# Optimization experiments

Measured on AMD Instinct MI355X. Metric: run time of the kernel, lower is better.

The kernel has to match this reference:

```python
import jax, jax.numpy as jnp
import numpy as np
import math

N_NODES = 50000
N_EDGES = 800000
D = 128
ALPHA = 0.1
BETA = 0.5


def setup_inputs() -> dict:
    key = jax.random.key(0)
    k = jax.random.split(key, 7)
    h = jax.random.normal(k[0], (N_NODES, D), dtype=jnp.float32)
    h0 = jax.random.normal(k[1], (N_NODES, D), dtype=jnp.float32)
    edge_row = jnp.sort(jax.random.randint(k[2], (N_EDGES,), 0, N_NODES, dtype=jnp.int32))
    edge_col = jax.random.randint(k[3], (N_EDGES,), 0, N_NODES, dtype=jnp.int32)
    edge_vals = jax.random.uniform(k[4], (N_EDGES,), dtype=jnp.float32)
    # nn.Linear(input_dim, output_dim): W is [out, in], b is [out]
    bound = 1.0 / math.sqrt(D)
    W = jax.random.uniform(k[5], (D, D), minval=-bound, maxval=bound, dtype=jnp.float32)
    b = jax.random.uniform(k[6], (D,), minval=-bound, maxval=bound, dtype=jnp.float32)
    return {"h": h, "h0": h0, "edge_row": edge_row, "edge_col": edge_col,
            "edge_vals": edge_vals, "W": W, "b": b, "l": 4}


def reference(h, h0, edge_row, edge_col, edge_vals, W, b, l):
    theta = math.log(BETA / l + 1.0)
    # sparse adj @ h : gather source features, scale by edge value, scatter-add to rows
    msgs = edge_vals[:, None] * h[edge_col]          # [E, D]
    hi = jax.ops.segment_sum(msgs, edge_row, num_segments=N_NODES)  # [N, D]
    support = (1.0 - ALPHA) * hi + ALPHA * h0
    lin = support @ W.T + b
    return theta * lin + (1.0 - theta) * support
```

## Files before the change

### kernel.cpp

```cpp
#include <hip/hip_runtime.h>
#include <hip/hip_bf16.h>
#include <math.h>

#define NN 50000
#define DD 128
#define ALPHA 0.1f
#define BETA 0.5f

typedef __attribute__((ext_vector_type(8))) short short8;
typedef __attribute__((ext_vector_type(4))) float floatx4;
typedef _Float16 h2 __attribute__((ext_vector_type(2)));

__device__ __forceinline__ float bf16lo(unsigned u) {
    return __uint_as_float(u << 16);
}
__device__ __forceinline__ float bf16hi(unsigned u) {
    return __uint_as_float(u & 0xffff0000u);
}
__device__ __forceinline__ unsigned pkh(float a, float b) {
    h2 p = {(_Float16)a, (_Float16)b};
    return __builtin_bit_cast(unsigned, p);
}
__device__ __forceinline__ h2 as_h2(unsigned u) {
    return __builtin_bit_cast(h2, u);
}

__global__ __launch_bounds__(256) void prep_kernel(
    const int* __restrict__ edge_row, int E, int* __restrict__ rp,
    const float* __restrict__ h, ushort* __restrict__ hh,
    const float* __restrict__ W, ushort* __restrict__ wf)
{
    const int t = blockIdx.x * 256 + threadIdx.x;

    if (hh != nullptr && t < NN * DD / 8) {
        const float4 v0 = *reinterpret_cast<const float4*>(h + (size_t)t * 8);
        const float4 v1 = *reinterpret_cast<const float4*>(h + (size_t)t * 8 + 4);
        uint4 o;
        o.x = pkh(v0.x, v0.y);
        o.y = pkh(v0.z, v0.w);
        o.z = pkh(v1.x, v1.y);
        o.w = pkh(v1.z, v1.w);
        *reinterpret_cast<uint4*>(hh + (size_t)t * 8) = o;
    }

    if (wf != nullptr && t < DD * DD / 4) {
        const float4 v = *reinterpret_cast<const float4*>(W + (size_t)t * 4);
        uint2 of;
        of.x = pkh(v.x, v.y);
        of.y = pkh(v.z, v.w);
        *reinterpret_cast<uint2*>(wf + (size_t)t * 4) = of;
    }

    if (t <= E) {
        if (t == 0) {
            int r0 = edge_row[0];
            for (int r = 0; r <= r0; ++r) rp[r] = 0;
        } else if (t == E) {
            int rl = edge_row[E - 1];
            for (int r = rl + 1; r <= NN; ++r) rp[r] = E;
        } else {
            int rprev = edge_row[t - 1];
            int rcur  = edge_row[t];
            for (int r = rprev + 1; r <= rcur; ++r) rp[r] = t;
        }
    }
}

__global__ __launch_bounds__(1024, 8) void fused16w(
    const ushort* __restrict__ hh, const float* __restrict__ h0,
    const int* __restrict__ edge_col, const float* __restrict__ edge_vals,
    const int* __restrict__ rp, const ushort* __restrict__ wf,
    const float* __restrict__ b, const int* __restrict__ lptr,
    float* __restrict__ out)
{
    __shared__ ushort sA[16][136];

    const int tid  = threadIdx.x;
    const int wave = tid >> 6;
    const int lane = tid & 63;
    const int g    = lane >> 4;
    const int li   = lane & 15;
    const int r0   = blockIdx.x * 16;
    const int r    = r0 + wave;

    const int lv = *lptr;
    const float theta  = logf(BETA / (float)lv + 1.0f);
    const float mtheta = 1.0f - theta;

    const int e0 = rp[r], e1 = rp[r + 1];

    h2 a0 = {0, 0}, a1 = {0, 0}, a2 = {0, 0}, a3 = {0, 0};

    for (int eb = e0; eb < e1; eb += 16) {
        #pragma unroll
        for (int u = 0; u < 4; ++u) {
            const int e  = eb + u * 4 + g;
            const int ee = min(e, e1 - 1);
            const int   c = edge_col[ee];
            const float v = (e < e1) ? edge_vals[ee] : 0.0f;
            const uint4 hv = *reinterpret_cast<const uint4*>(
                hh + (size_t)c * DD + li * 8);
            const _Float16 vh = (_Float16)v;
            const h2 vv = {vh, vh};
            a0 += as_h2(hv.x) * vv;
            a1 += as_h2(hv.y) * vv;
            a2 += as_h2(hv.z) * vv;
            a3 += as_h2(hv.w) * vv;
        }
    }

    float acc[8];
    acc[0] = (float)a0.x; acc[1] = (float)a0.y;
    acc[2] = (float)a1.x; acc[3] = (float)a1.y;
    acc[4] = (float)a2.x; acc[5] = (float)a2.y;
    acc[6] = (float)a3.x; acc[7] = (float)a3.y;

    #pragma unroll
    for (int j = 0; j < 8; ++j) {
        acc[j] += __shfl_xor(acc[j], 16);
        acc[j] += __shfl_xor(acc[j], 32);
    }

    if (g == 0) {
        const float4 h0a = *reinterpret_cast<const float4*>(
            h0 + (size_t)r * DD + li * 8);
        const float4 h0b = *reinterpret_cast<const float4*>(
            h0 + (size_t)r * DD + li * 8 + 4);
        float sup[8];
        sup[0] = fmaf(1.0f - ALPHA, acc[0], ALPHA * h0a.x);
        sup[1] = fmaf(1.0f - ALPHA, acc[1], ALPHA * h0a.y);
        sup[2] = fmaf(1.0f - ALPHA, acc[2], ALPHA * h0a.z);
        sup[3] = fmaf(1.0f - ALPHA, acc[3], ALPHA * h0a.w);
        sup[4] = fmaf(1.0f - ALPHA, acc[4], ALPHA * h0b.x);
        sup[5] = fmaf(1.0f - ALPHA, acc[5], ALPHA * h0b.y);
        sup[6] = fmaf(1.0f - ALPHA, acc[6], ALPHA * h0b.z);
        sup[7] = fmaf(1.0f - ALPHA, acc[7], ALPHA * h0b.w);
        uint4 pk;
        pk.x = pkh(sup[0], sup[1]);
        pk.y = pkh(sup[2], sup[3]);
        pk.z = pkh(sup[4], sup[5]);
        pk.w = pkh(sup[6], sup[7]);
        *reinterpret_cast<uint4*>(&sA[wave][li * 8]) = pk;
    }
    __syncthreads();

    if (wave >= 8) return;

    const int la = lane & 15;
    const int k0 = (lane >> 4) * 8;
    const int c  = wave * 16 + la;

    floatx4 facc = (floatx4){0.f, 0.f, 0.f, 0.f};

    #pragma unroll
    for (int s = 0; s < 4; ++s) {
        const int k = s * 32 + k0;
        const short8 af = *reinterpret_cast<const short8*>(&sA[la][k]);
        const short8 bf = *reinterpret_cast<const short8*>(
            wf + (size_t)c * DD + k);
        facc = __builtin_amdgcn_mfma_f32_16x16x32_f16(af, bf, facc, 0, 0, 0);
    }

    const int rg = (lane >> 4) * 4;
    const float bb = b[c];
    #pragma unroll
    for (int j = 0; j < 4; ++j) {
        const int rl = rg + j;
        const float sup = (float)(*reinterpret_cast<const _Float16*>(&sA[rl][c]));
        out[(size_t)(r0 + rl) * DD + c] =
            theta * (facc[j] + bb) + mtheta * sup;
    }
}

__global__ __launch_bounds__(256, 6) void agg_fp32(
    const float* __restrict__ h, const float* __restrict__ h0,
    const int* __restrict__ edge_col, const float* __restrict__ edge_vals,
    const int* __restrict__ rp, float* __restrict__ io)
{
    const int wave = threadIdx.x >> 6;
    const int lane = threadIdx.x & 63;
    const int p    = lane >> 5;
    const int li   = lane & 31;
    const int r    = blockIdx.x * 4 + wave;
    if (r >= NN) return;

    const int e0 = rp[r], e1 = rp[r + 1];

    float4 A[4];
    #pragma unroll
    for (int u = 0; u < 4; ++u) A[u] = make_float4(0.f, 0.f, 0.f, 0.f);

    for (int eb = e0; eb < e1; eb += 8) {
        #pragma unroll
        for (int u = 0; u < 4; ++u) {
            const int e  = eb + 2 * u + p;
            const int ee = min(e, e1 - 1);
            const int   c = edge_col[ee];
            const float v = (e < e1) ? edge_vals[ee] : 0.0f;
            const float4 hv =
                *reinterpret_cast<const float4*>(h + (size_t)c * DD + li * 4);
            A[u].x = fmaf(v, hv.x, A[u].x);
            A[u].y = fmaf(v, hv.y, A[u].y);
            A[u].z = fmaf(v, hv.z, A[u].z);
            A[u].w = fmaf(v, hv.w, A[u].w);
        }
    }
    float4 s;
    s.x = (A[0].x + A[1].x) + (A[2].x + A[3].x);
    s.y = (A[0].y + A[1].y) + (A[2].y + A[3].y);
    s.z = (A[0].z + A[1].z) + (A[2].z + A[3].z);
    s.w = (A[0].w + A[1].w) + (A[2].w + A[3].w);
    s.x += __shfl_xor(s.x, 32);
    s.y += __shfl_xor(s.y, 32);
    s.z += __shfl_xor(s.z, 32);
    s.w += __shfl_xor(s.w, 32);

    if (p == 0) {
        const float4 h0v =
            *reinterpret_cast<const float4*>(h0 + (size_t)r * DD + li * 4);
        float4 sup;
        sup.x = fmaf(1.0f - ALPHA, s.x, ALPHA * h0v.x);
        sup.y = fmaf(1.0f - ALPHA, s.y, ALPHA * h0v.y);
        sup.z = fmaf(1.0f - ALPHA, s.z, ALPHA * h0v.z);
        sup.w = fmaf(1.0f - ALPHA, s.w, ALPHA * h0v.w);
        *reinterpret_cast<float4*>(io + (size_t)r * DD + li * 4) = sup;
    }
}

#define RPB 64
#define SPAD 132
#define WPAD 136

__global__ __launch_bounds__(512, 4) void lin_kernel(
    float* io, const float* __restrict__ W, const float* __restrict__ b,
    const int* __restrict__ lptr)
{
    __shared__ float sS[RPB][SPAD];
    __shared__ __hip_bfloat16 sWt[DD][WPAD];

    const int tid = threadIdx.x;
    const int r0  = blockIdx.x * RPB;
    const int tr  = tid >> 4;
    const int tc  = tid & 15;

    const int lv = *lptr;
    const float theta  = logf(BETA / (float)lv + 1.0f);
    const float mtheta = 1.0f - theta;

    for (int i = tid * 4; i < DD * DD; i += 512 * 4) {
        const float4 w4 = *reinterpret_cast<const float4*>(W + i);
        const int o = i >> 7;
        const int k = i & 127;
        sWt[k + 0][o] = __float2bfloat16(w4.x);
        sWt[k + 1][o] = __float2bfloat16(w4.y);
        sWt[k + 2][o] = __float2bfloat16(w4.z);
        sWt[k + 3][o] = __float2bfloat16(w4.w);
    }

    for (int idx = tid; idx < RPB * 32; idx += 512) {
        const int row = idx >> 5;
        const int q   = idx & 31;
        const int rr  = r0 + row;
        const float4 v = (rr < NN)
            ? *reinterpret_cast<const float4*>(io + (size_t)rr * DD + q * 4)
            : make_float4(0.f, 0.f, 0.f, 0.f);
        *reinterpret_cast<float4*>(&sS[row][q * 4]) = v;
    }
    __syncthreads();

    float acc[2][8];
    #pragma unroll
    for (int i = 0; i < 2; ++i)
        #pragma unroll
        for (int j = 0; j < 8; ++j) acc[i][j] = 0.f;

    for (int k = 0; k < DD; k += 4) {
        const float4 a0 = *reinterpret_cast<const float4*>(&sS[tr * 2 + 0][k]);
        const float4 a1 = *reinterpret_cast<const float4*>(&sS[tr * 2 + 1][k]);
        const float aa0[4] = {a0.x, a0.y, a0.z, a0.w};
        const float aa1[4] = {a1.x, a1.y, a1.z, a1.w};
        #pragma unroll
        for (int kk = 0; kk < 4; ++kk) {
            const uint4 wr = *reinterpret_cast<const uint4*>(&sWt[k + kk][tc * 8]);
            float w[8];
            w[0] = bf16lo(wr.x); w[1] = bf16hi(wr.x);
            w[2] = bf16lo(wr.y); w[3] = bf16hi(wr.y);
            w[4] = bf16lo(wr.z); w[5] = bf16hi(wr.z);
            w[6] = bf16lo(wr.w); w[7] = bf16hi(wr.w);
            #pragma unroll
            for (int j = 0; j < 8; ++j) {
                acc[0][j] = fmaf(aa0[kk], w[j], acc[0][j]);
                acc[1][j] = fmaf(aa1[kk], w[j], acc[1][j]);
            }
        }
    }

    #pragma unroll
    for (int i = 0; i < 2; ++i) {
        const int ri = tr * 2 + i;
        const int rr = r0 + ri;
        if (rr >= NN) continue;
        #pragma unroll
        for (int j4 = 0; j4 < 2; ++j4) {
            const int cc = tc * 8 + j4 * 4;
            const float4 bv  = *reinterpret_cast<const float4*>(&b[cc]);
            const float4 sup = *reinterpret_cast<const float4*>(&sS[ri][cc]);
            float4 o4;
            o4.x = theta * (acc[i][j4 * 4 + 0] + bv.x) + mtheta * sup.x;
            o4.y = theta * (acc[i][j4 * 4 + 1] + bv.y) + mtheta * sup.y;
            o4.z = theta * (acc[i][j4 * 4 + 2] + bv.z) + mtheta * sup.z;
            o4.w = theta * (acc[i][j4 * 4 + 3] + bv.w) + mtheta * sup.w;
            *reinterpret_cast<float4*>(io + (size_t)rr * DD + cc) = o4;
        }
    }
}

extern "C" void kernel_launch(void* const* d_in, const int* in_sizes, int n_in,
                              void* d_out, int out_size, void* d_ws, size_t ws_size,
                              hipStream_t stream) {
    const float* h         = (const float*)d_in[0];
    const float* h0        = (const float*)d_in[1];
    const int*   edge_row  = (const int*)d_in[2];
    const int*   edge_col  = (const int*)d_in[3];
    const float* edge_vals = (const float*)d_in[4];
    const float* W         = (const float*)d_in[5];
    const float* b         = (const float*)d_in[6];
    const int*   lptr      = (const int*)d_in[7];
    const int E = in_sizes[2];

    char* wsb = (char*)d_ws;
    const size_t sz_hh = (size_t)NN * DD * sizeof(ushort);
    const size_t sz_w  = (size_t)DD * DD * sizeof(ushort);
    int*    rp = (int*)wsb;
    ushort* hh = (ushort*)(wsb + (1 << 18));
    ushort* wf = (ushort*)(wsb + (1 << 18) + sz_hh);
    float*  io = (float*)d_out;

    const size_t need = (size_t)(1 << 18) + sz_hh + sz_w;

    const int nT = (NN * DD / 8 > E + 1) ? NN * DD / 8 : E + 1;
    const int gridP = (nT + 255) / 256;

    if (ws_size >= need) {
        prep_kernel<<<gridP, 256, 0, stream>>>(edge_row, E, rp, h, hh, W, wf);
        fused16w<<<NN / 16, 1024, 0, stream>>>(
            hh, h0, edge_col, edge_vals, rp, wf, b, lptr, io);
    } else {
        prep_kernel<<<gridP, 256, 0, stream>>>(edge_row, E, rp, h,
                                               nullptr, W, nullptr);
        agg_fp32<<<(NN + 3) / 4, 256, 0, stream>>>(h, h0, edge_col, edge_vals, rp, io);
        lin_kernel<<<(NN + RPB - 1) / RPB, 512, 0, stream>>>(io, W, b, lptr);
    }
}
```

Measured before the change: 66.46 us.

## Process two rows per wave in fused aggregation kernel with 512-thread blocks

Changes the fused SpMM+linear kernel from 16 waves per block (one row each) to 8 waves per block with each wave aggregating two rows at once. This interleaves the gather loads for two rows to raise memory-level parallelism per wave. It also removes the idle half of the block during the MFMA phase, since all 8 waves now do the GEMM. The trade-off is load imbalance between paired rows: the loop runs to the longer of the two edge lists. It also uses more registers per wave.

```diff
diff --git a/kernel.cpp b/kernel.cpp
--- a/kernel.cpp
+++ b/kernel.cpp
@@ -66,7 +66,7 @@
     }
 }
 
-__global__ __launch_bounds__(1024, 8) void fused16w(
+__global__ __launch_bounds__(512, 8) void fused8w(
     const ushort* __restrict__ hh, const float* __restrict__ h0,
     const int* __restrict__ edge_col, const float* __restrict__ edge_vals,
     const int* __restrict__ rp, const ushort* __restrict__ wf,
@@ -81,70 +81,114 @@
     const int g    = lane >> 4;
     const int li   = lane & 15;
     const int r0   = blockIdx.x * 16;
-    const int r    = r0 + wave;
+    const int rA   = r0 + wave * 2;
+    const int rB   = rA + 1;
 
     const int lv = *lptr;
     const float theta  = logf(BETA / (float)lv + 1.0f);
     const float mtheta = 1.0f - theta;
 
-    const int e0 = rp[r], e1 = rp[r + 1];
-
-    h2 a0 = {0, 0}, a1 = {0, 0}, a2 = {0, 0}, a3 = {0, 0};
-
-    for (int eb = e0; eb < e1; eb += 16) {
+    const int e0A = rp[rA], e1A = rp[rA + 1];
+    const int e0B = rp[rB], e1B = rp[rB + 1];
+
+    h2 aA0 = {0, 0}, aA1 = {0, 0}, aA2 = {0, 0}, aA3 = {0, 0};
+    h2 aB0 = {0, 0}, aB1 = {0, 0}, aB2 = {0, 0}, aB3 = {0, 0};
+
+    for (int ebA = e0A, ebB = e0B; ebA < e1A || ebB < e1B;
+         ebA += 16, ebB += 16) {
         #pragma unroll
         for (int u = 0; u < 4; ++u) {
-            const int e  = eb + u * 4 + g;
-            const int ee = min(e, e1 - 1);
-            const int   c = edge_col[ee];
-            const float v = (e < e1) ? edge_vals[ee] : 0.0f;
-            const uint4 hv = *reinterpret_cast<const uint4*>(
-                hh + (size_t)c * DD + li * 8);
-            const _Float16 vh = (_Float16)v;
-            const h2 vv = {vh, vh};
-            a0 += as_h2(hv.x) * vv;
-            a1 += as_h2(hv.y) * vv;
-            a2 += as_h2(hv.z) * vv;
-            a3 += as_h2(hv.w) * vv;
-        }
-    }
-
-    float acc[8];
-    acc[0] = (float)a0.x; acc[1] = (float)a0.y;
-    acc[2] = (float)a1.x; acc[3] = (float)a1.y;
-    acc[4] = (float)a2.x; acc[5] = (float)a2.y;
-    acc[6] = (float)a3.x; acc[7] = (float)a3.y;
+            const int eA  = ebA + u * 4 + g;
+            const int eeA = max(min(eA, e1A - 1), 0);
+            const int cA  = edge_col[eeA];
+            const float vA = (eA < e1A) ? edge_vals[eeA] : 0.0f;
+            const uint4 hvA = *reinterpret_cast<const uint4*>(
+                hh + (size_t)cA * DD + li * 8);
+
+            const int eB  = ebB + u * 4 + g;
+            const int eeB = max(min(eB, e1B - 1), 0);
+            const int cB  = edge_col[eeB];
+            const float vB = (eB < e1B) ? edge_vals[eeB] : 0.0f;
+            const uint4 hvB = *reinterpret_cast<const uint4*>(
+                hh + (size_t)cB * DD + li * 8);
+
+            const _Float16 vhA = (_Float16)vA;
+            const h2 vvA = {vhA, vhA};
+            aA0 += as_h2(hvA.x) * vvA;
+            aA1 += as_h2(hvA.y) * vvA;
+            aA2 += as_h2(hvA.z) * vvA;
+            aA3 += as_h2(hvA.w) * vvA;
+
+            const _Float16 vhB = (_Float16)vB;
+            const h2 vvB = {vhB, vhB};
+            aB0 += as_h2(hvB.x) * vvB;
+            aB1 += as_h2(hvB.y) * vvB;
+            aB2 += as_h2(hvB.z) * vvB;
+            aB3 += as_h2(hvB.w) * vvB;
+        }
+    }
+
+    float accA[8], accB[8];
+    accA[0] = (float)aA0.x; accA[1] = (float)aA0.y;
+    accA[2] = (float)aA1.x; accA[3] = (float)aA1.y;
+    accA[4] = (float)aA2.x; accA[5] = (float)aA2.y;
+    accA[6] = (float)aA3.x; accA[7] = (float)aA3.y;
+    accB[0] = (float)aB0.x; accB[1] = (float)aB0.y;
+    accB[2] = (float)aB1.x; accB[3] = (float)aB1.y;
+    accB[4] = (float)aB2.x; accB[5] = (float)aB2.y;
+    accB[6] = (float)aB3.x; accB[7] = (float)aB3.y;
 
     #pragma unroll
     for (int j = 0; j < 8; ++j) {
-        acc[j] += __shfl_xor(acc[j], 16);
-        acc[j] += __shfl_xor(acc[j], 32);
+        accA[j] += __shfl_xor(accA[j], 16);
+        accA[j] += __shfl_xor(accA[j], 32);
+        accB[j] += __shfl_xor(accB[j], 16);
+        accB[j] += __shfl_xor(accB[j], 32);
     }
 
     if (g == 0) {
-        const float4 h0a = *reinterpret_cast<const float4*>(
-            h0 + (size_t)r * DD + li * 8);
-        const float4 h0b = *reinterpret_cast<const float4*>(
-            h0 + (size_t)r * DD + li * 8 + 4);
-        float sup[8];
-        sup[0] = fmaf(1.0f - ALPHA, acc[0], ALPHA * h0a.x);
-        sup[1] = fmaf(1.0f - ALPHA, acc[1], ALPHA * h0a.y);
-        sup[2] = fmaf(1.0f - ALPHA, acc[2], ALPHA * h0a.z);
-        sup[3] = fmaf(1.0f - ALPHA, acc[3], ALPHA * h0a.w);
-        sup[4] = fmaf(1.0f - ALPHA, acc[4], ALPHA * h0b.x);
-        sup[5] = fmaf(1.0f - ALPHA, acc[5], ALPHA * h0b.y);
-        sup[6] = fmaf(1.0f - ALPHA, acc[6], ALPHA * h0b.z);
-        sup[7] = fmaf(1.0f - ALPHA, acc[7], ALPHA * h0b.w);
-        uint4 pk;
-        pk.x = pkh(sup[0], sup[1]);
-        pk.y = pkh(sup[2], sup[3]);
-        pk.z = pkh(sup[4], sup[5]);
-        pk.w = pkh(sup[6], sup[7]);
-        *reinterpret_cast<uint4*>(&sA[wave][li * 8]) = pk;
+        {
+            const float4 h0a = *reinterpret_cast<const float4*>(
+                h0 + (size_t)rA * DD + li * 8);
+            const float4 h0b = *reinterpret_cast<const float4*>(
+                h0 + (size_t)rA * DD + li * 8 + 4);
+            float s0 = fmaf(1.0f - ALPHA, accA[0], ALPHA * h0a.x);
+            float s1 = fmaf(1.0f - ALPHA, accA[1], ALPHA * h0a.y);
+            float s2 = fmaf(1.0f - ALPHA, accA[2], ALPHA * h0a.z);
+            float s3 = fmaf(1.0f - ALPHA, accA[3], ALPHA * h0a.w);
+            float s4 = fmaf(1.0f - ALPHA, accA[4], ALPHA * h0b.x);
+            float s5 = fmaf(1.0f - ALPHA, accA[5], ALPHA * h0b.y);
+            float s6 = fmaf(1.0f - ALPHA, accA[6], ALPHA * h0b.z);
+            float s7 = fmaf(1.0f - ALPHA, accA[7], ALPHA * h0b.w);
+            uint4 pk;
+            pk.x = pkh(s0, s1);
+            pk.y = pkh(s2, s3);
+            pk.z = pkh(s4, s5);
+            pk.w = pkh(s6, s7);
+            *reinterpret_cast<uint4*>(&sA[wave * 2][li * 8]) = pk;
+        }
+        {
+            const float4 h0a = *reinterpret_cast<const float4*>(
+                h0 + (size_t)rB * DD + li * 8);
+            const float4 h0b = *reinterpret_cast<const float4*>(
+                h0 + (size_t)rB * DD + li * 8 + 4);
+            float s0 = fmaf(1.0f - ALPHA, accB[0], ALPHA * h0a.x);
+            float s1 = fmaf(1.0f - ALPHA, accB[1], ALPHA * h0a.y);
+            float s2 = fmaf(1.0f - ALPHA, accB[2], ALPHA * h0a.z);
+            float s3 = fmaf(1.0f - ALPHA, accB[3], ALPHA * h0a.w);
+            float s4 = fmaf(1.0f - ALPHA, accB[4], ALPHA * h0b.x);
+            float s5 = fmaf(1.0f - ALPHA, accB[5], ALPHA * h0b.y);
+            float s6 = fmaf(1.0f - ALPHA, accB[6], ALPHA * h0b.z);
+            float s7 = fmaf(1.0f - ALPHA, accB[7], ALPHA * h0b.w);
+            uint4 pk;
+            pk.x = pkh(s0, s1);
+            pk.y = pkh(s2, s3);
+            pk.z = pkh(s4, s5);
+            pk.w = pkh(s6, s7);
+            *reinterpret_cast<uint4*>(&sA[wave * 2 + 1][li * 8]) = pk;
+        }
     }
     __syncthreads();
-
-    if (wave >= 8) return;
 
     const int la = lane & 15;
     const int k0 = (lane >> 4) * 8;
@@ -343,7 +387,7 @@
 
     if (ws_size >= need) {
         prep_kernel<<<gridP, 256, 0, stream>>>(edge_row, E, rp, h, hh, W, wf);
-        fused16w<<<NN / 16, 1024, 0, stream>>>(
+        fused8w<<<NN / 16, 512, 0, stream>>>(
             hh, h0, edge_col, edge_vals, rp, wf, b, lptr, io);
     } else {
         prep_kernel<<<gridP, 256, 0, stream>>>(edge_row, E, rp, h,
```

After: 67.06 us. About the same (+0.9%).
